# Performance work log

Hardware: AMD Instinct MI355X
Metric: run time of the kernel (lower is better)

The kernel has to match this reference:

```python
import jax, jax.numpy as jnp
import numpy as np

DIM = 8          # per-head dim
ATT_EPS = 1e-15  # LiteMLA eps
BN_EPS = 1e-5    # torch BatchNorm2d default eps


def conv2d(x, w, groups=1, pad=0):
    # x: NCHW, w: OIHW
    return jax.lax.conv_general_dilated(
        x, w, window_strides=(1, 1), padding=[(pad, pad), (pad, pad)],
        dimension_numbers=('NCHW', 'OIHW', 'NCHW'), feature_group_count=groups)


def setup_inputs() -> dict:
    key = jax.random.key(0)
    ks = jax.random.split(key, 6)
    B, C, H, W = 4, 128, 128, 128
    heads = C // DIM            # 16
    t3 = 3 * C                  # 3*total_dim = 384
    x = jax.random.normal(ks[0], (B, C, H, W), jnp.float32)
    w_qkv = jax.random.normal(ks[1], (t3, C, 1, 1), jnp.float32) * 0.02
    w_dw = jax.random.normal(ks[2], (t3, 1, 5, 5), jnp.float32) * 0.02      # depthwise 5x5
    w_pw = jax.random.normal(ks[3], (t3, t3 // (3 * heads), 1, 1), jnp.float32) * 0.05  # grouped 1x1, groups=3*heads
    w_proj = jax.random.normal(ks[4], (C, 2 * C, 1, 1), jnp.float32) * 0.02  # proj 1x1: 2C -> C
    bn_gamma = jnp.ones((C,), jnp.float32)
    bn_beta = jnp.zeros((C,), jnp.float32)
    bn_mean = jnp.zeros((C,), jnp.float32)
    bn_var = jnp.ones((C,), jnp.float32)
    return dict(x=x, w_qkv=w_qkv, w_dw=w_dw, w_pw=w_pw, w_proj=w_proj,
                bn_gamma=bn_gamma, bn_beta=bn_beta, bn_mean=bn_mean, bn_var=bn_var)


def reference(x, w_qkv, w_dw, w_pw, w_proj, bn_gamma, bn_beta, bn_mean, bn_var):
    # qkv: 1x1 conv, no norm / no act
    qkv = conv2d(x, w_qkv)                                  # (B, 3C, H, W)
    t3 = w_qkv.shape[0]
    # aggreg[0]: depthwise 5x5 + grouped 1x1
    groups_pw = t3 // w_pw.shape[1]                         # 3*heads
    agg = conv2d(conv2d(qkv, w_dw, groups=t3, pad=2), w_pw, groups=groups_pw)
    qkv = jnp.concatenate([qkv, agg], axis=1)               # (B, 6C, H, W)

    B, _, H, W = qkv.shape
    N = H * W
    qkv = qkv.reshape(B, -1, 3 * DIM, N)                    # (B, 2*heads, 3*dim, N)
    q = jax.nn.relu(qkv[:, :, :DIM])                        # (B, h, d, N)
    k = jax.nn.relu(qkv[:, :, DIM:2 * DIM])                 # (B, h, d, N)
    v = qkv[:, :, 2 * DIM:]                                 # (B, h, d, N)
    # pad v with a row of ones for normalization
    v = jnp.concatenate([v, jnp.ones_like(v[:, :, :1])], axis=2)  # (B, h, d+1, N)

    vk = jnp.einsum('bhdn,bhen->bhde', v, k)                # (B, h, d+1, d)
    out = jnp.einsum('bhde,bhen->bhdn', vk, q)              # (B, h, d+1, N)
    out = out[:, :, :-1] / (out[:, :, -1:] + ATT_EPS)       # (B, h, d, N)
    out = out.reshape(B, -1, H, W)                          # (B, 2C, H, W)

    # proj: 1x1 conv + BatchNorm2d (inference), no act
    out = conv2d(out, w_proj)                               # (B, C, H, W)
    inv = bn_gamma / jnp.sqrt(bn_var + BN_EPS)
    out = out * inv[:, None, None] + (bn_beta - bn_mean * inv)[:, None, None]
    return out
```

## Files before the change

### kernel.cpp

```cpp
#include <hip/hip_runtime.h>

#define BB 4
#define CIN 128
#define T3 384
#define HH 128
#define WW 128
#define NPIX 16384
#define QKV_ELE (BB*T3*NPIX)
#define NCHUNK 16

#define SEC 4160
#define KGP 1040
#define PLN 520

typedef __attribute__((ext_vector_type(8))) short bf16x8;
typedef __attribute__((ext_vector_type(4))) float f32x4;

__device__ __forceinline__ unsigned splitpack(float x) {
  unsigned u = __float_as_uint(x);
  unsigned hb = (u + 0x7fffu + ((u >> 16) & 1u)) >> 16;
  float lo = x - __uint_as_float(hb << 16);
  unsigned ul = __float_as_uint(lo);
  unsigned lb = (ul + 0x7fffu + ((ul >> 16) & 1u)) >> 16;
  return (hb << 16) | (lb & 0xffffu);
}

__device__ __forceinline__ void packpair(float a, float b, unsigned& hi, unsigned& lo) {
  unsigned p0 = splitpack(a), p1 = splitpack(b);
  hi = (p1 & 0xffff0000u) | (p0 >> 16);
  lo = (p1 << 16) | (p0 & 0xffffu);
}

__global__ __launch_bounds__(256) void k0_wprep(const float* __restrict__ wqkv,
                                                unsigned* __restrict__ wimg,
                                                float* __restrict__ zbuf) {
  int id = blockIdx.x * 256 + threadIdx.x;
  if (id < 16) zbuf[id] = 0.f;
  int i = id & 3;
  int co = (id >> 2) & 127;
  int kgrp = (id >> 9) & 3;
  int c = (id >> 11) & 3;
  int m = id >> 13;
  int ci = c * 32 + kgrp * 8 + 2 * i;
  const float* wrow = wqkv + (size_t)(m * 128 + co) * 128 + ci;
  unsigned hi, lo;
  packpair(wrow[0], wrow[1], hi, lo);
  size_t base = (size_t)(m * 4 + c) * SEC + kgrp * KGP + co * 4 + i;
  wimg[base] = hi;
  wimg[base + PLN] = lo;
}

__global__ __launch_bounds__(256) void k1_qkv_mfma(const float* __restrict__ x,
                                                   const unsigned* __restrict__ wimg,
                                                   float* __restrict__ qkv) {
  __shared__ __align__(16) unsigned Xp[4 * KGP];
  __shared__ __align__(16) unsigned Wp[4 * KGP];
  const int t = threadIdx.x;
  const int p = blockIdx.x;
  const int qd = p / 24;
  const int r_ = p - qd * 24;
  const int m = r_ >> 3;
  const int tt = qd * 8 + (r_ & 7);
  const int n0 = (tt & 127) * 128;
  const int b = tt >> 7;
  const float* xb = x + (size_t)b * CIN * NPIX + n0;

  const int l = t & 63;
  const int w = t >> 6;
  const int g = l >> 4;
  const int lc = l & 15;
  const int ch = w >> 1;
  const int nh = w & 1;

  const int kg = t >> 6;
  const int nn_ = t & 63;

  f32x4 acc[4][4];
  #pragma unroll
  for (int i = 0; i < 4; ++i)
    #pragma unroll
    for (int j = 0; j < 4; ++j) acc[i][j] = (f32x4){0.f, 0.f, 0.f, 0.f};

  for (int c = 0; c < 4; ++c) {
    {
      const uint4* wsrc = (const uint4*)(wimg + (size_t)(m * 4 + c) * SEC);
      uint4* wdst = (uint4*)Wp;
      #pragma unroll
      for (int r = 0; r < 5; ++r) {
        int idx = t + r * 256;
        if (idx < 1040) wdst[idx] = wsrc[idx];
      }
    }
    {
      const float* colbase = xb + (size_t)(c * 32 + kg * 8) * NPIX;
      #pragma unroll
      for (int half = 0; half < 2; ++half) {
        int n = nn_ + half * 64;
        const float* colp = colbase + n;
        unsigned hp[4], lp[4];
        #pragma unroll
        for (int i = 0; i < 4; ++i)
          packpair(colp[(size_t)(2 * i) * NPIX], colp[(size_t)(2 * i + 1) * NPIX],
                   hp[i], lp[i]);
        *(uint4*)&Xp[kg * KGP + n * 4] = make_uint4(hp[0], hp[1], hp[2], hp[3]);
        *(uint4*)&Xp[kg * KGP + PLN + n * 4] = make_uint4(lp[0], lp[1], lp[2], lp[3]);
      }
    }
    __syncthreads();

    bf16x8 bh[4], bl[4];
    #pragma unroll
    for (int ng = 0; ng < 4; ++ng) {
      const int nb = (nh * 64 + ng * 16 + lc) * 4;
      bh[ng] = *(const bf16x8*)&Xp[g * KGP + nb];
      bl[ng] = *(const bf16x8*)&Xp[g * KGP + PLN + nb];
    }
    #pragma unroll
    for (int cg = 0; cg < 4; ++cg) {
      const int cb = (ch * 64 + cg * 16 + lc) * 4;
      bf16x8 ah = *(const bf16x8*)&Wp[g * KGP + cb];
      bf16x8 al = *(const bf16x8*)&Wp[g * KGP + PLN + cb];
      #pragma unroll
      for (int ng = 0; ng < 4; ++ng) {
        acc[cg][ng] = __builtin_amdgcn_mfma_f32_16x16x32_bf16(ah, bh[ng], acc[cg][ng], 0, 0, 0);
        acc[cg][ng] = __builtin_amdgcn_mfma_f32_16x16x32_bf16(ah, bl[ng], acc[cg][ng], 0, 0, 0);
        acc[cg][ng] = __builtin_amdgcn_mfma_f32_16x16x32_bf16(al, bh[ng], acc[cg][ng], 0, 0, 0);
      }
    }
    __syncthreads();
  }
  #pragma unroll
  for (int cg = 0; cg < 4; ++cg) {
    const size_t corow = (size_t)b * T3 + m * 128 + ch * 64 + cg * 16 + g * 4;
    #pragma unroll
    for (int ng = 0; ng < 4; ++ng) {
      const int nn = n0 + nh * 64 + ng * 16 + lc;
      #pragma unroll
      for (int rr = 0; rr < 4; ++rr)
        qkv[(corow + rr) * NPIX + nn] = acc[cg][ng][rr];
    }
  }
}

#define PDW 36
__global__ __launch_bounds__(256, 2) void k2_dwpw(const float* __restrict__ qkv,
                                                  const float* __restrict__ wdw,
                                                  const float* __restrict__ wpw,
                                                  const float* __restrict__ zbuf,
                                                  float* __restrict__ agg) {
  __shared__ __align__(16) float dws[8 * 16 * PDW];
  __shared__ float wds[8][25];
  __shared__ float wps[64];
  const int t = threadIdx.x;
  const int p = blockIdx.x;
  const int L = (p & 7) * 768 + (p >> 3);
  const int z = L >> 5;
  const int rem = L & 31;
  const int x0 = (rem & 3) * 32;
  const int y0 = (rem >> 2) * 16;
  const int b = z / 48;
  const int g = z % 48;
  const float* src = qkv + ((size_t)b * T3 + g * 8) * NPIX;

  for (int idx = t; idx < 200; idx += 256)
    wds[idx / 25][idx % 25] = wdw[(size_t)g * 200 + idx];
  if (t < 64) wps[t] = wpw[g * 64 + t];
  __syncthreads();

  const int ch = t >> 5;
  const int xq = t & 7;
  const int yg = (t >> 3) & 3;
  const float* plane = src + (size_t)ch * NPIX;
  const int gx0 = x0 + 4 * xq - 4;
  const bool ex0 = (gx0 >= 0);
  const bool ex2 = (gx0 + 11 < WW);

  f32x4 u[8][3];
  #pragma unroll
  for (int r = 0; r < 8; ++r) {
    const int gy = y0 + 4 * yg - 2 + r;
    const bool iny = (unsigned)gy < (unsigned)HH;
    const float* rp = plane + gy * WW + gx0;
    const float* p0 = (iny && ex0) ? rp : zbuf;
    const float* p1 = iny ? (rp + 4) : zbuf;
    const float* p2 = (iny && ex2) ? (rp + 8) : zbuf;
    u[r][0] = *(const f32x4*)p0;
    u[r][1] = *(const f32x4*)p1;
    u[r][2] = *(const f32x4*)p2;
  }

  float dacc[4][4];
  #pragma unroll
  for (int jy = 0; jy < 4; ++jy)
    #pragma unroll
    for (int jx = 0; jx < 4; ++jx) dacc[jy][jx] = 0.f;

  #pragma unroll
  for (int r = 0; r < 8; ++r) {
    float vals[12] = {u[r][0][0], u[r][0][1], u[r][0][2], u[r][0][3],
                      u[r][1][0], u[r][1][1], u[r][1][2], u[r][1][3],
                      u[r][2][0], u[r][2][1], u[r][2][2], u[r][2][3]};
    #pragma unroll
    for (int jy = 0; jy < 4; ++jy) {
      int ky = r - jy;
      if (ky < 0 || ky > 4) continue;
      #pragma unroll
      for (int kx = 0; kx < 5; ++kx) {
        float wv = wds[ch][ky * 5 + kx];
        #pragma unroll
        for (int jx = 0; jx < 4; ++jx)
          dacc[jy][jx] += wv * vals[jx + kx + 2];
      }
    }
  }

  #pragma unroll
  for (int jy = 0; jy < 4; ++jy) {
    float4 o = make_float4(dacc[jy][0], dacc[jy][1], dacc[jy][2], dacc[jy][3]);
    *(float4*)&dws[ch * (16 * PDW) + (yg * 4 + jy) * PDW + xq * 4] = o;
  }
  __syncthreads();

  float* dst = agg + ((size_t)b * T3 + g * 8) * NPIX + (size_t)y0 * WW + x0;
  #pragma unroll
  for (int pp = 0; pp < 2; ++pp) {
    int pix = t + pp * 256;
    int py = pix >> 5;
    int px = pix & 31;
    float dv[8];
    #pragma unroll
    for (int ic = 0; ic < 8; ++ic) dv[ic] = dws[ic * (16 * PDW) + py * PDW + px];
    #pragma unroll
    for (int oc = 0; oc < 8; ++oc) {
      float s = 0.f;
      #pragma unroll
      for (int ic = 0; ic < 8; ++ic) s += wps[oc * 8 + ic] * dv[ic];
      dst[(size_t)oc * NPIX + py * WW + px] = s;
    }
  }
}

__global__ __launch_bounds__(256) void k3_vk(const float* __restrict__ qkv,
                                             const float* __restrict__ agg,
                                             float* __restrict__ part) {
  const int chunk = blockIdx.x;
  const int bh = blockIdx.y;
  const int b = bh >> 5;
  const int h = bh & 31;
  const int hh = h & 15;
  const float* base = (h < 16 ? qkv : agg) + ((size_t)b * T3 + hh * 24) * NPIX;
  const float* kb = base + 8 * NPIX;
  const float* vb = base + 16 * NPIX;
  const int t = threadIdx.x;
  const int wv = t >> 6;
  const int lane = t & 63;
  const int d0 = wv * 2;

  float accA[8], accB[8], accS[8];
  #pragma unroll
  for (int e = 0; e < 8; ++e) { accA[e] = 0.f; accB[e] = 0.f; accS[e] = 0.f; }

  int p = chunk * (NPIX / NCHUNK) + lane;
  for (int it = 0; it < (NPIX / NCHUNK / 64); ++it, p += 64) {
    float kvv[8];
    #pragma unroll
    for (int e = 0; e < 8; ++e) kvv[e] = fmaxf(kb[(size_t)e * NPIX + p], 0.f);
    float vA = vb[(size_t)d0 * NPIX + p];
    float vB = vb[(size_t)(d0 + 1) * NPIX + p];
    #pragma unroll
    for (int e = 0; e < 8; ++e) { accA[e] += vA * kvv[e]; accB[e] += vB * kvv[e]; }
    if (wv == 0) {
      #pragma unroll
      for (int e = 0; e < 8; ++e) accS[e] += kvv[e];
    }
  }
  #pragma unroll
  for (int e = 0; e < 8; ++e) {
    #pragma unroll
    for (int m = 1; m < 64; m <<= 1) {
      accA[e] += __shfl_xor(accA[e], m);
      accB[e] += __shfl_xor(accB[e], m);
    }
  }
  if (wv == 0) {
    #pragma unroll
    for (int e = 0; e < 8; ++e)
      #pragma unroll
      for (int m = 1; m < 64; m <<= 1) accS[e] += __shfl_xor(accS[e], m);
  }
  if (lane == 0) {
    float* pr = part + ((size_t)bh * NCHUNK + chunk) * 72;
    #pragma unroll
    for (int e = 0; e < 8; ++e) {
      pr[d0 * 8 + e] = accA[e];
      pr[(d0 + 1) * 8 + e] = accB[e];
    }
    if (wv == 0) {
      #pragma unroll
      for (int e = 0; e < 8; ++e) pr[64 + e] = accS[e];
    }
  }
}

__global__ __launch_bounds__(128) void k3b_sum(const float* __restrict__ part,
                                               float* __restrict__ vk) {
  const int bh = blockIdx.x;
  const int j = threadIdx.x;
  if (j < 72) {
    float s = 0.f;
    #pragma unroll
    for (int c = 0; c < NCHUNK; ++c) s += part[((size_t)bh * NCHUNK + c) * 72 + j];
    vk[(size_t)bh * 72 + j] = s;
  }
}

__global__ __launch_bounds__(256) void k3c_M(const float* __restrict__ wproj,
                                             const float* __restrict__ vk,
                                             const float* __restrict__ gamma,
                                             const float* __restrict__ beta,
                                             const float* __restrict__ mean,
                                             const float* __restrict__ var,
                                             unsigned* __restrict__ Mimg,
                                             float* __restrict__ shiftb) {
  int id = blockIdx.x * 256 + threadIdx.x;
  int i = id & 3;
  int co = (id >> 2) & 127;
  int kgrp = (id >> 9) & 3;
  int cidx = (id >> 11) & 7;
  int b = id >> 14;
  int h = cidx * 4 + kgrp;
  float inv = gamma[co] * rsqrtf(var[co] + 1e-5f);
  const float* wrow = wproj + (size_t)co * 256 + h * 8;
  const float* vkc = vk + ((size_t)b * 32 + h) * 72;
  float s0 = 0.f, s1 = 0.f;
  #pragma unroll
  for (int d = 0; d < 8; ++d) {
    float wv = wrow[d];
    s0 += wv * vkc[d * 8 + 2 * i];
    s1 += wv * vkc[d * 8 + 2 * i + 1];
  }
  unsigned hi, lo;
  packpair(inv * s0, inv * s1, hi, lo);
  size_t base = (size_t)(b * 8 + cidx) * SEC + kgrp * KGP + co * 4 + i;
  Mimg[base] = hi;
  Mimg[base + PLN] = lo;
  if (b == 0 && cidx == 0 && kgrp == 0 && i == 0)
    shiftb[co] = beta[co] - mean[co] * inv;
}

__global__ __launch_bounds__(256) void k4_mfma(const float* __restrict__ qkv,
                                               const float* __restrict__ agg,
                                               const float* __restrict__ vk,
                                               const unsigned* __restrict__ Mimg,
                                               const float* __restrict__ shiftb,
                                               float* __restrict__ out) {
  __shared__ __align__(16) unsigned Ap[4 * KGP];
  __shared__ __align__(16) unsigned Bp[4 * KGP];
  const int t = threadIdx.x;
  const int n0 = blockIdx.x * 128;
  const int b = blockIdx.y;

  const int l = t & 63;
  const int w = t >> 6;
  const int g = l >> 4;
  const int lc = l & 15;
  const int ch = w >> 1;
  const int nh = w & 1;

  const int hj = t >> 6;
  const int nn_ = t & 63;

  f32x4 acc[4][4];
  #pragma unroll
  for (int i = 0; i < 4; ++i)
    #pragma unroll
    for (int j = 0; j < 4; ++j) acc[i][j] = (f32x4){0.f, 0.f, 0.f, 0.f};

  for (int cidx = 0; cidx < 8; ++cidx) {
    {
      const uint4* asrc = (const uint4*)(Mimg + (size_t)(b * 8 + cidx) * SEC);
      uint4* adst = (uint4*)Ap;
      #pragma unroll
      for (int r = 0; r < 5; ++r) {
        int idx = t + r * 256;
        if (idx < 1040) adst[idx] = asrc[idx];
      }
    }
    {
      const int h = cidx * 4 + hj;
      const float* srcb = (h < 16 ? qkv : agg) +
                          ((size_t)b * T3 + (h & 15) * 24) * NPIX + n0;
      const float* vkr = vk + ((size_t)b * 32 + h) * 72 + 64;
      float vv[8];
      #pragma unroll
      for (int e = 0; e < 8; ++e) vv[e] = vkr[e];
      #pragma unroll
      for (int half = 0; half < 2; ++half) {
        int n = nn_ + half * 64;
        float q[8];
        float den = 1e-15f;
        #pragma unroll
        for (int e = 0; e < 8; ++e) {
          q[e] = fmaxf(srcb[(size_t)e * NPIX + n], 0.f);
          den += vv[e] * q[e];
        }
        float rd = 1.0f / den;
        unsigned hp[4], lp[4];
        #pragma unroll
        for (int i = 0; i < 4; ++i)
          packpair(q[2 * i] * rd, q[2 * i + 1] * rd, hp[i], lp[i]);
        *(uint4*)&Bp[hj * KGP + n * 4] = make_uint4(hp[0], hp[1], hp[2], hp[3]);
        *(uint4*)&Bp[hj * KGP + PLN + n * 4] = make_uint4(lp[0], lp[1], lp[2], lp[3]);
      }
    }
    __syncthreads();

    bf16x8 bh[4], bl[4];
    #pragma unroll
    for (int ng = 0; ng < 4; ++ng) {
      const int nb = (nh * 64 + ng * 16 + lc) * 4;
      bh[ng] = *(const bf16x8*)&Bp[g * KGP + nb];
      bl[ng] = *(const bf16x8*)&Bp[g * KGP + PLN + nb];
    }
    #pragma unroll
    for (int cg = 0; cg < 4; ++cg) {
      const int cb = (ch * 64 + cg * 16 + lc) * 4;
      bf16x8 ah = *(const bf16x8*)&Ap[g * KGP + cb];
      bf16x8 al = *(const bf16x8*)&Ap[g * KGP + PLN + cb];
      #pragma unroll
      for (int ng = 0; ng < 4; ++ng) {
        acc[cg][ng] = __builtin_amdgcn_mfma_f32_16x16x32_bf16(ah, bh[ng], acc[cg][ng], 0, 0, 0);
        acc[cg][ng] = __builtin_amdgcn_mfma_f32_16x16x32_bf16(ah, bl[ng], acc[cg][ng], 0, 0, 0);
        acc[cg][ng] = __builtin_amdgcn_mfma_f32_16x16x32_bf16(al, bh[ng], acc[cg][ng], 0, 0, 0);
      }
    }
    __syncthreads();
  }
  #pragma unroll
  for (int cg = 0; cg < 4; ++cg) {
    const int cobase = ch * 64 + cg * 16 + g * 4;
    #pragma unroll
    for (int ng = 0; ng < 4; ++ng) {
      const int nn = n0 + nh * 64 + ng * 16 + lc;
      #pragma unroll
      for (int rr = 0; rr < 4; ++rr) {
        int co = cobase + rr;
        out[((size_t)b * 128 + co) * NPIX + nn] = acc[cg][ng][rr] + shiftb[co];
      }
    }
  }
}

__global__ void fill_sentinel(float* o, int n) {
  int i = blockIdx.x * 256 + threadIdx.x;
  if (i < n) o[i] = 12345.0f;
}

extern "C" void kernel_launch(void* const* d_in, const int* in_sizes, int n_in,
                              void* d_out, int out_size, void* d_ws, size_t ws_size,
                              hipStream_t stream) {
  const float* x     = (const float*)d_in[0];
  const float* wqkv  = (const float*)d_in[1];
  const float* wdw   = (const float*)d_in[2];
  const float* wpw   = (const float*)d_in[3];
  const float* wproj = (const float*)d_in[4];
  const float* gamma = (const float*)d_in[5];
  const float* beta  = (const float*)d_in[6];
  const float* mean  = (const float*)d_in[7];
  const float* var   = (const float*)d_in[8];
  float* out = (float*)d_out;
  float* ws = (float*)d_ws;

  const size_t partF = 128 * NCHUNK * 72;
  const size_t mimgF = 32 * SEC;
  const size_t wimgF = 12 * SEC;
  const size_t needF = (size_t)QKV_ELE * 2 + partF + 9216 + 128 + mimgF + wimgF + 16;
  if (ws_size < needF * 4) {
    fill_sentinel<<<dim3((out_size + 255) / 256), dim3(256), 0, stream>>>(out, out_size);
    return;
  }
  float* qkv    = ws;
  float* agg    = qkv + QKV_ELE;
  float* part   = agg + QKV_ELE;
  float* vkbuf  = part + partF;
  float* shiftb = vkbuf + 9216;
  unsigned* Mimg = (unsigned*)(shiftb + 128);
  unsigned* wimg = Mimg + mimgF;
  float* zbuf   = (float*)(wimg + wimgF);

  k0_wprep<<<dim3(96), 256, 0, stream>>>(wqkv, wimg, zbuf);
  k1_qkv_mfma<<<dim3(1536), 256, 0, stream>>>(x, wimg, qkv);
  k2_dwpw<<<dim3(6144), 256, 0, stream>>>(qkv, wdw, wpw, zbuf, agg);
  k3_vk<<<dim3(NCHUNK, 128), 256, 0, stream>>>(qkv, agg, part);
  k3b_sum<<<dim3(128), 128, 0, stream>>>(part, vkbuf);
  k3c_M<<<dim3(256), 256, 0, stream>>>(wproj, vkbuf, gamma, beta, mean, var, Mimg, shiftb);
  k4_mfma<<<dim3(128, 4), 256, 0, stream>>>(qkv, agg, vkbuf, Mimg, shiftb, out);
}
```

Baseline: 143.4 us.

## Fuse depthwise/pointwise aggregation with vk reduction per head tile

Merges the depthwise+grouped-pointwise kernel and the vk reduction kernel into one kernel. Each block now handles one head (24 channels) over a 32x16 tile. It computes the aggregated k and v in shared memory and reduces vk for them directly, without a global round-trip. It also reduces vk for the raw qkv k/v of the same tile from staged tiles, then writes the aggregated q channels. This removes re-reading qkv/agg in a separate reduction pass and drops one launch, at the cost of more shared memory, more syncs and fewer, heavier blocks. It also skips writing aggregated k/v to global, which is fine only if the final kernel does not read them.

```diff
diff --git a/kernel.cpp b/kernel.cpp
--- a/kernel.cpp
+++ b/kernel.cpp
@@ -7,7 +7,6 @@
 #define WW 128
 #define NPIX 16384
 #define QKV_ELE (BB*T3*NPIX)
-#define NCHUNK 16
 
 #define SEC 4160
 #define KGP 1040
@@ -71,7 +70,6 @@
   const int lc = l & 15;
   const int ch = w >> 1;
   const int nh = w & 1;
-
   const int kg = t >> 6;
   const int nn_ = t & 63;
 
@@ -143,38 +141,15 @@
 }
 
 #define PDW 36
-__global__ __launch_bounds__(256, 2) void k2_dwpw(const float* __restrict__ qkv,
-                                                  const float* __restrict__ wdw,
-                                                  const float* __restrict__ wpw,
-                                                  const float* __restrict__ zbuf,
-                                                  float* __restrict__ agg) {
-  __shared__ __align__(16) float dws[8 * 16 * PDW];
-  __shared__ float wds[8][25];
-  __shared__ float wps[64];
-  const int t = threadIdx.x;
-  const int p = blockIdx.x;
-  const int L = (p & 7) * 768 + (p >> 3);
-  const int z = L >> 5;
-  const int rem = L & 31;
-  const int x0 = (rem & 3) * 32;
-  const int y0 = (rem >> 2) * 16;
-  const int b = z / 48;
-  const int g = z % 48;
-  const float* src = qkv + ((size_t)b * T3 + g * 8) * NPIX;
-
-  for (int idx = t; idx < 200; idx += 256)
-    wds[idx / 25][idx % 25] = wdw[(size_t)g * 200 + idx];
-  if (t < 64) wps[t] = wpw[g * 64 + t];
-  __syncthreads();
-
-  const int ch = t >> 5;
-  const int xq = t & 7;
-  const int yg = (t >> 3) & 3;
-  const float* plane = src + (size_t)ch * NPIX;
+
+__device__ __forceinline__ void dw_compute(const float* __restrict__ plane,
+                                           const float* __restrict__ w25,
+                                           const float* __restrict__ zbuf,
+                                           int x0, int y0, int xq, int yg,
+                                           float dacc[4][4]) {
   const int gx0 = x0 + 4 * xq - 4;
   const bool ex0 = (gx0 >= 0);
   const bool ex2 = (gx0 + 11 < WW);
-
   f32x4 u[8][3];
   #pragma unroll
   for (int r = 0; r < 8; ++r) {
@@ -188,13 +163,10 @@
     u[r][1] = *(const f32x4*)p1;
     u[r][2] = *(const f32x4*)p2;
   }
-
-  float dacc[4][4];
   #pragma unroll
   for (int jy = 0; jy < 4; ++jy)
     #pragma unroll
     for (int jx = 0; jx < 4; ++jx) dacc[jy][jx] = 0.f;
-
   #pragma unroll
   for (int r = 0; r < 8; ++r) {
     float vals[12] = {u[r][0][0], u[r][0][1], u[r][0][2], u[r][0][3],
@@ -206,72 +178,37 @@
       if (ky < 0 || ky > 4) continue;
       #pragma unroll
       for (int kx = 0; kx < 5; ++kx) {
-        float wv = wds[ch][ky * 5 + kx];
+        float wv = w25[ky * 5 + kx];
         #pragma unroll
         for (int jx = 0; jx < 4; ++jx)
           dacc[jy][jx] += wv * vals[jx + kx + 2];
       }
     }
   }
-
-  #pragma unroll
-  for (int jy = 0; jy < 4; ++jy) {
-    float4 o = make_float4(dacc[jy][0], dacc[jy][1], dacc[jy][2], dacc[jy][3]);
-    *(float4*)&dws[ch * (16 * PDW) + (yg * 4 + jy) * PDW + xq * 4] = o;
-  }
-  __syncthreads();
-
-  float* dst = agg + ((size_t)b * T3 + g * 8) * NPIX + (size_t)y0 * WW + x0;
-  #pragma unroll
-  for (int pp = 0; pp < 2; ++pp) {
-    int pix = t + pp * 256;
-    int py = pix >> 5;
-    int px = pix & 31;
-    float dv[8];
-    #pragma unroll
-    for (int ic = 0; ic < 8; ++ic) dv[ic] = dws[ic * (16 * PDW) + py * PDW + px];
-    #pragma unroll
-    for (int oc = 0; oc < 8; ++oc) {
-      float s = 0.f;
-      #pragma unroll
-      for (int ic = 0; ic < 8; ++ic) s += wps[oc * 8 + ic] * dv[ic];
-      dst[(size_t)oc * NPIX + py * WW + px] = s;
-    }
-  }
-}
-
-__global__ __launch_bounds__(256) void k3_vk(const float* __restrict__ qkv,
-                                             const float* __restrict__ agg,
-                                             float* __restrict__ part) {
-  const int chunk = blockIdx.x;
-  const int bh = blockIdx.y;
-  const int b = bh >> 5;
-  const int h = bh & 31;
-  const int hh = h & 15;
-  const float* base = (h < 16 ? qkv : agg) + ((size_t)b * T3 + hh * 24) * NPIX;
-  const float* kb = base + 8 * NPIX;
-  const float* vb = base + 16 * NPIX;
-  const int t = threadIdx.x;
+}
+
+__device__ __forceinline__ void vk_reduce(const float* __restrict__ kb,
+                                          const float* __restrict__ vb,
+                                          float* __restrict__ pr, int t) {
   const int wv = t >> 6;
   const int lane = t & 63;
   const int d0 = wv * 2;
-
   float accA[8], accB[8], accS[8];
   #pragma unroll
   for (int e = 0; e < 8; ++e) { accA[e] = 0.f; accB[e] = 0.f; accS[e] = 0.f; }
-
-  int p = chunk * (NPIX / NCHUNK) + lane;
-  for (int it = 0; it < (NPIX / NCHUNK / 64); ++it, p += 64) {
-    float kvv[8];
-    #pragma unroll
-    for (int e = 0; e < 8; ++e) kvv[e] = fmaxf(kb[(size_t)e * NPIX + p], 0.f);
-    float vA = vb[(size_t)d0 * NPIX + p];
-    float vB = vb[(size_t)(d0 + 1) * NPIX + p];
-    #pragma unroll
-    for (int e = 0; e < 8; ++e) { accA[e] += vA * kvv[e]; accB[e] += vB * kvv[e]; }
+  #pragma unroll
+  for (int it = 0; it < 8; ++it) {
+    int p = it * 64 + lane;
+    float kv[8];
+    #pragma unroll
+    for (int e = 0; e < 8; ++e) kv[e] = kb[e * 512 + p];
+    float vA = vb[d0 * 512 + p];
+    float vB = vb[(d0 + 1) * 512 + p];
+    #pragma unroll
+    for (int e = 0; e < 8; ++e) { accA[e] += vA * kv[e]; accB[e] += vB * kv[e]; }
     if (wv == 0) {
       #pragma unroll
-      for (int e = 0; e < 8; ++e) accS[e] += kvv[e];
+      for (int e = 0; e < 8; ++e) accS[e] += kv[e];
     }
   }
   #pragma unroll
@@ -289,7 +226,6 @@
       for (int m = 1; m < 64; m <<= 1) accS[e] += __shfl_xor(accS[e], m);
   }
   if (lane == 0) {
-    float* pr = part + ((size_t)bh * NCHUNK + chunk) * 72;
     #pragma unroll
     for (int e = 0; e < 8; ++e) {
       pr[d0 * 8 + e] = accA[e];
@@ -302,14 +238,152 @@
   }
 }
 
-__global__ __launch_bounds__(128) void k3b_sum(const float* __restrict__ part,
+__global__ __launch_bounds__(256, 2) void k2_fused(const float* __restrict__ qkv,
+                                                   const float* __restrict__ wdw,
+                                                   const float* __restrict__ wpw,
+                                                   const float* __restrict__ zbuf,
+                                                   float* __restrict__ agg,
+                                                   float* __restrict__ part2) {
+  __shared__ __align__(16) float dwsv[8 * 16 * PDW];
+  __shared__ __align__(16) float kbuf[8 * 512];
+  __shared__ float wds[24][25];
+  __shared__ float wps[192];
+  const int t = threadIdx.x;
+  const int p = blockIdx.x;
+  const int L = (p & 7) * 256 + (p >> 3);
+  const int z = L >> 5;
+  const int rem = L & 31;
+  const int x0 = (rem & 3) * 32;
+  const int y0 = (rem >> 2) * 16;
+  const int b = z >> 4;
+  const int hh = z & 15;
+  const float* src = qkv + ((size_t)b * T3 + hh * 24) * NPIX;
+
+  for (int idx = t; idx < 600; idx += 256)
+    wds[idx / 25][idx % 25] = wdw[(size_t)hh * 600 + idx];
+  if (t < 192) wps[t] = wpw[hh * 192 + t];
+  __syncthreads();
+
+  const int ch = t >> 5;
+  const int xq = t & 7;
+  const int yg = (t >> 3) & 3;
+  float dacc[4][4];
+
+  dw_compute(src + (size_t)(8 + ch) * NPIX, &wds[8 + ch][0], zbuf, x0, y0, xq, yg, dacc);
+  #pragma unroll
+  for (int jy = 0; jy < 4; ++jy)
+    *(float4*)&dwsv[ch * (16 * PDW) + (yg * 4 + jy) * PDW + xq * 4] =
+        make_float4(dacc[jy][0], dacc[jy][1], dacc[jy][2], dacc[jy][3]);
+  __syncthreads();
+  #pragma unroll
+  for (int pp = 0; pp < 2; ++pp) {
+    int pix = t + pp * 256;
+    int py = pix >> 5, px = pix & 31;
+    float dv[8];
+    #pragma unroll
+    for (int ic = 0; ic < 8; ++ic) dv[ic] = dwsv[ic * (16 * PDW) + py * PDW + px];
+    #pragma unroll
+    for (int oc = 0; oc < 8; ++oc) {
+      float s = 0.f;
+      #pragma unroll
+      for (int ic = 0; ic < 8; ++ic) s += wps[64 + oc * 8 + ic] * dv[ic];
+      kbuf[oc * 512 + pix] = fmaxf(s, 0.f);
+    }
+  }
+  __syncthreads();
+
+  dw_compute(src + (size_t)(16 + ch) * NPIX, &wds[16 + ch][0], zbuf, x0, y0, xq, yg, dacc);
+  #pragma unroll
+  for (int jy = 0; jy < 4; ++jy)
+    *(float4*)&dwsv[ch * (16 * PDW) + (yg * 4 + jy) * PDW + xq * 4] =
+        make_float4(dacc[jy][0], dacc[jy][1], dacc[jy][2], dacc[jy][3]);
+  __syncthreads();
+  float vout[2][8];
+  #pragma unroll
+  for (int pp = 0; pp < 2; ++pp) {
+    int pix = t + pp * 256;
+    int py = pix >> 5, px = pix & 31;
+    float dv[8];
+    #pragma unroll
+    for (int ic = 0; ic < 8; ++ic) dv[ic] = dwsv[ic * (16 * PDW) + py * PDW + px];
+    #pragma unroll
+    for (int oc = 0; oc < 8; ++oc) {
+      float s = 0.f;
+      #pragma unroll
+      for (int ic = 0; ic < 8; ++ic) s += wps[128 + oc * 8 + ic] * dv[ic];
+      vout[pp][oc] = s;
+    }
+  }
+  __syncthreads();
+  #pragma unroll
+  for (int pp = 0; pp < 2; ++pp) {
+    int pix = t + pp * 256;
+    #pragma unroll
+    for (int oc = 0; oc < 8; ++oc) dwsv[oc * 512 + pix] = vout[pp][oc];
+  }
+  __syncthreads();
+
+  vk_reduce(kbuf, dwsv, part2 + ((size_t)(z * 2 + 1) * 32 + rem) * 72, t);
+  __syncthreads();
+
+  #pragma unroll
+  for (int j = 0; j < 8; ++j) {
+    int qd = t + j * 256;
+    int buf = qd >> 10;
+    int ch2 = (qd >> 7) & 7;
+    int r2 = qd & 127;
+    int py = r2 >> 3, qx = r2 & 7;
+    const float* gp = src + (size_t)(8 + buf * 8 + ch2) * NPIX + (y0 + py) * WW + x0 + qx * 4;
+    f32x4 v = *(const f32x4*)gp;
+    if (buf == 0) {
+      v[0] = fmaxf(v[0], 0.f); v[1] = fmaxf(v[1], 0.f);
+      v[2] = fmaxf(v[2], 0.f); v[3] = fmaxf(v[3], 0.f);
+      *(f32x4*)&kbuf[ch2 * 512 + py * 32 + qx * 4] = v;
+    } else {
+      *(f32x4*)&dwsv[ch2 * 512 + py * 32 + qx * 4] = v;
+    }
+  }
+  __syncthreads();
+
+  vk_reduce(kbuf, dwsv, part2 + ((size_t)(z * 2 + 0) * 32 + rem) * 72, t);
+  __syncthreads();
+
+  dw_compute(src + (size_t)ch * NPIX, &wds[ch][0], zbuf, x0, y0, xq, yg, dacc);
+  #pragma unroll
+  for (int jy = 0; jy < 4; ++jy)
+    *(float4*)&dwsv[ch * (16 * PDW) + (yg * 4 + jy) * PDW + xq * 4] =
+        make_float4(dacc[jy][0], dacc[jy][1], dacc[jy][2], dacc[jy][3]);
+  __syncthreads();
+  float* dst = agg + ((size_t)b * T3 + hh * 24) * NPIX + (size_t)y0 * WW + x0;
+  #pragma unroll
+  for (int pp = 0; pp < 2; ++pp) {
+    int pix = t + pp * 256;
+    int py = pix >> 5, px = pix & 31;
+    float dv[8];
+    #pragma unroll
+    for (int ic = 0; ic < 8; ++ic) dv[ic] = dwsv[ic * (16 * PDW) + py * PDW + px];
+    #pragma unroll
+    for (int oc = 0; oc < 8; ++oc) {
+      float s = 0.f;
+      #pragma unroll
+      for (int ic = 0; ic < 8; ++ic) s += wps[oc * 8 + ic] * dv[ic];
+      dst[(size_t)oc * NPIX + py * WW + px] = s;
+    }
+  }
+}
+
+__global__ __launch_bounds__(128) void k3b_sum(const float* __restrict__ part2,
                                                float* __restrict__ vk) {
   const int bh = blockIdx.x;
   const int j = threadIdx.x;
   if (j < 72) {
+    int b = bh >> 5, h = bh & 31;
+    int z = b * 16 + (h & 15);
+    int ph = h >> 4;
+    const float* srcp = part2 + ((size_t)(z * 2 + ph) * 32) * 72 + j;
     float s = 0.f;
     #pragma unroll
-    for (int c = 0; c < NCHUNK; ++c) s += part[((size_t)bh * NCHUNK + c) * 72 + j];
+    for (int c = 0; c < 32; ++c) s += srcp[(size_t)c * 72];
     vk[(size_t)bh * 72 + j] = s;
   }
 }
@@ -366,7 +440,6 @@
   const int lc = l & 15;
   const int ch = w >> 1;
   const int nh = w & 1;
-
   const int hj = t >> 6;
   const int nn_ = t & 63;
 
@@ -471,18 +544,18 @@
   float* out = (float*)d_out;
   float* ws = (float*)d_ws;
 
-  const size_t partF = 128 * NCHUNK * 72;
+  const size_t part2F = 64 * 2 * 32 * 72;
   const size_t mimgF = 32 * SEC;
   const size_t wimgF = 12 * SEC;
-  const size_t needF = (size_t)QKV_ELE * 2 + partF + 9216 + 128 + mimgF + wimgF + 16;
+  const size_t needF = (size_t)QKV_ELE * 2 + part2F + 9216 + 128 + mimgF + wimgF + 16;
   if (ws_size < needF * 4) {
     fill_sentinel<<<dim3((out_size + 255) / 256), dim3(256), 0, stream>>>(out, out_size);
     return;
   }
   float* qkv    = ws;
   float* agg    = qkv + QKV_ELE;
-  float* part   = agg + QKV_ELE;
-  float* vkbuf  = part + partF;
+  float* part2  = agg + QKV_ELE;
+  float* vkbuf  = part2 + part2F;
   float* shiftb = vkbuf + 9216;
   unsigned* Mimg = (unsigned*)(shiftb + 128);
   unsigned* wimg = Mimg + mimgF;
@@ -490,9 +563,8 @@
 
   k0_wprep<<<dim3(96), 256, 0, stream>>>(wqkv, wimg, zbuf);
   k1_qkv_mfma<<<dim3(1536), 256, 0, stream>>>(x, wimg, qkv);
-  k2_dwpw<<<dim3(6144), 256, 0, stream>>>(qkv, wdw, wpw, zbuf, agg);
-  k3_vk<<<dim3(NCHUNK, 128), 256, 0, stream>>>(qkv, agg, part);
-  k3b_sum<<<dim3(128), 128, 0, stream>>>(part, vkbuf);
+  k2_fused<<<dim3(2048), 256, 0, stream>>>(qkv, wdw, wpw, zbuf, agg, part2);
+  k3b_sum<<<dim3(128), 128, 0, stream>>>(part2, vkbuf);
   k3c_M<<<dim3(256), 256, 0, stream>>>(wproj, vkbuf, gamma, beta, mean, var, Mimg, shiftb);
   k4_mfma<<<dim3(128, 4), 256, 0, stream>>>(qkv, agg, vkbuf, Mimg, shiftb, out);
 }
```

After: 146.5 us. 2.2% more time.
